# Optimization experiments

Measured on AMD Instinct MI355X. Metric: run time of the kernel, lower is better.

## Reference

```python
import jax, jax.numpy as jnp
import numpy as np

K, L = 9, 32


def conv1d(x, w):
    # x: [b, C, P], w: [O, C, 3]; padding=1 kernel=3 == SAME
    return jax.lax.conv_general_dilated(
        x, w, window_strides=(1,), padding='SAME',
        dimension_numbers=('NCH', 'OIH', 'NCH'))


def prior_surface(x, w1, w2, w3, w4):
    # x: [b, P]
    h = jax.nn.relu(conv1d(x[:, None, :], w1))
    h = jax.nn.relu(conv1d(h, w2))
    h = jax.nn.relu(conv1d(h, w3))
    out = x[:, None, :] + jax.nn.relu(conv1d(h, w4))
    return jnp.clip(out, 0.0, 1.0)[:, 0, :]


def setup_inputs() -> dict:
    key = jax.random.key(0)
    ks = jax.random.split(key, 9)
    b, E, M, P = 32, 20, 64, 3072
    d_split = 0.1 * jax.random.normal(ks[0], (b, E, M), jnp.float32)
    surf0 = jax.random.uniform(ks[1], (b, P), dtype=jnp.float32)
    clouds0 = jax.random.uniform(ks[2], (b, E, P), dtype=jnp.float32)
    # scale Phi so gradients stay in a sane range for the [0,1] clamps
    Phi_split = jax.random.normal(ks[3], (b, E, M, P), jnp.float32) / P
    rho_base = 0.1 * jax.random.uniform(ks[4], (b,), dtype=jnp.float32)
    rho = jnp.ones((K,), jnp.float32)

    def kaiming(k, shape):
        fan_in = shape[-2] * shape[-1]
        return jax.random.normal(k, shape, jnp.float32) * np.float32(np.sqrt(2.0 / fan_in))

    w1 = kaiming(ks[5], (K, L, 1, 3))
    w2 = kaiming(ks[6], (K, L, L, 3))
    w3 = kaiming(ks[7], (K, L, L, 3))
    w4 = kaiming(ks[8], (K, 1, L, 3))
    return {"d_split": d_split, "surf0": surf0, "clouds0": clouds0,
            "Phi_split": Phi_split, "rho_base": rho_base, "rho": rho,
            "w1": w1, "w2": w2, "w3": w3, "w4": w4, "n_epochs": 20}


def reference(d_split, surf0, clouds0, Phi_split, rho_base, rho, w1, w2, w3, w4, n_epochs):
    # d_split: [b,E,M], surf0: [b,P], clouds0: [b,E,P], Phi_split: [b,E,M,P], rho_base: [b]
    surf, clouds = surf0, clouds0
    out_surface, out_clouds = [], []
    for i in range(K):
        t0 = 1.0 - clouds                       # [b,E,P]
        t1 = t0 * t0
        tmp = clouds + t1 * surf[:, None, :]    # [b,E,P]
        y = jnp.einsum('bemp,bep->bem', Phi_split, tmp)          # Phi @ tmp
        t2 = jnp.einsum('bemp,bem->bep', Phi_split, y - d_split)  # PhiT @ resid
        # the torch loop over j accumulates grad_surf += 2*t2*t1; equivalent sum over E
        grad_surf = surf0 + 2.0 * jnp.sum(t2 * t1, axis=1)        # [b,P]
        grad_clouds = 2.0 * t2 - 4.0 * t2 * surf[:, None, :] * t0 # [b,E,P]
        rho_i = jnp.clip(rho[i], 0.1, 3.0)
        r_surf = surf - rho_base[:, None] * rho_i * grad_surf
        r_clouds = clouds - rho_base[:, None, None] * rho_i * grad_clouds
        surf = prior_surface(r_surf, w1[i], w2[i], w3[i], w4[i])
        clouds = jax.nn.relu(r_clouds)
        out_surface.append(surf)
        out_clouds.append(clouds)
    return (surf, clouds, jnp.stack(out_surface), jnp.stack(out_clouds))
```

## Files before the change

kernel.cpp:

```cpp
#include <hip/hip_runtime.h>

#define B_ 32
#define E_ 20
#define M_ 64
#define P_ 3072
#define K_ 9
#define TT 384
#define NT (P_ / TT)

#define PHI_SCALE 65536.0f
#define PHI_INV   (1.0f / 65536.0f)

typedef float floatx2 __attribute__((ext_vector_type(2)));

__device__ __forceinline__ unsigned int pack4_fp8(float f0, float f1, float f2, float f3)
{
    int w = 0;
    w = __builtin_amdgcn_cvt_pk_fp8_f32(f0, f1, w, false);
    w = __builtin_amdgcn_cvt_pk_fp8_f32(f2, f3, w, true);
    return (unsigned int)w;
}

template <int MODE>
__global__ __launch_bounds__(256) void k_y(
    const float* __restrict__ PhiF,
    const unsigned char* __restrict__ Phi8,
    unsigned char* __restrict__ Phi8out,
    const float* __restrict__ dsplit,
    const float* __restrict__ surf_cur,
    const float* __restrict__ clouds_cur,
    float* __restrict__ yr)
{
    __shared__ float s_tmp[P_];
    const int bid = blockIdx.x >> 1;
    const int mh  = blockIdx.x & 1;
    const int b   = bid / E_;
    const int tid = threadIdx.x;

    const float4* cl4 = reinterpret_cast<const float4*>(clouds_cur + (size_t)bid * P_);
    const float4* sf4 = reinterpret_cast<const float4*>(surf_cur + (size_t)b * P_);
    for (int f = tid; f < P_ / 4; f += 256) {
        float4 c4 = cl4[f], s4 = sf4[f], tm;
        float t0x = 1.f - c4.x, t0y = 1.f - c4.y, t0z = 1.f - c4.z, t0w = 1.f - c4.w;
        tm.x = c4.x + t0x * t0x * s4.x;
        tm.y = c4.y + t0y * t0y * s4.y;
        tm.z = c4.z + t0z * t0z * s4.z;
        tm.w = c4.w + t0w * t0w * s4.w;
        reinterpret_cast<float4*>(s_tmp)[f] = tm;
    }
    __syncthreads();

    const int wave = tid >> 6, lane = tid & 63;
    const size_t base = (size_t)bid * (M_ * P_);

    #pragma unroll
    for (int r = 0; r < 8; ++r) {
        const int mg = mh * 32 + wave * 8 + r;
        float acc = 0.f;
        if constexpr (MODE != 2) {
            const float4* prow = reinterpret_cast<const float4*>(PhiF + base + (size_t)mg * P_);
            unsigned int* orow = reinterpret_cast<unsigned int*>(Phi8out + base + (size_t)mg * P_);
            #pragma unroll
            for (int j = 0; j < 12; ++j) {
                const int f = j * 64 + lane;
                float4 v = prow[f];
                float4 t = reinterpret_cast<const float4*>(s_tmp)[f];
                acc += v.x * t.x + v.y * t.y + v.z * t.z + v.w * t.w;
                if constexpr (MODE == 1) {
                    orow[f] = pack4_fp8(v.x * PHI_SCALE, v.y * PHI_SCALE,
                                        v.z * PHI_SCALE, v.w * PHI_SCALE);
                }
            }
        } else {
            const uint2* prow = reinterpret_cast<const uint2*>(Phi8 + base + (size_t)mg * P_);
            #pragma unroll
            for (int j = 0; j < 6; ++j) {
                const int f = j * 64 + lane;
                uint2 w = prow[f];
                floatx2 l0 = __builtin_amdgcn_cvt_pk_f32_fp8((int)w.x, false);
                floatx2 h0 = __builtin_amdgcn_cvt_pk_f32_fp8((int)w.x, true);
                floatx2 l1 = __builtin_amdgcn_cvt_pk_f32_fp8((int)w.y, false);
                floatx2 h1 = __builtin_amdgcn_cvt_pk_f32_fp8((int)w.y, true);
                float4 a = reinterpret_cast<const float4*>(s_tmp)[2 * f];
                float4 bb = reinterpret_cast<const float4*>(s_tmp)[2 * f + 1];
                acc += l0.x * a.x + l0.y * a.y + h0.x * a.z + h0.y * a.w
                     + l1.x * bb.x + l1.y * bb.y + h1.x * bb.z + h1.y * bb.w;
            }
        }
        #pragma unroll
        for (int off = 32; off > 0; off >>= 1)
            acc += __shfl_down(acc, off, 64);
        if (lane == 0) {
            if constexpr (MODE == 2) acc *= PHI_INV;
            yr[bid * M_ + mg] = acc - dsplit[bid * M_ + mg];
        }
    }
}

__global__ __launch_bounds__(192) void k_t2_f8(
    const unsigned char* __restrict__ Phi8,
    const float* __restrict__ yr,
    const float* __restrict__ surf_cur,
    const float* __restrict__ clouds_cur,
    const float* __restrict__ rho_base,
    const float* __restrict__ rho_i,
    float* __restrict__ s2t1,
    float* __restrict__ out_clouds_i)
{
    __shared__ float s_yr[M_];
    const int bid = blockIdx.x >> 1;
    const int ph  = blockIdx.x & 1;
    const int b   = bid / E_;
    const int tid = threadIdx.x;

    if (tid < M_) s_yr[tid] = yr[bid * M_ + tid];
    __syncthreads();

    const int p0 = ph * 1536 + tid * 8;
    const unsigned char* phi = Phi8 + (size_t)bid * (M_ * P_) + p0;

    float acc[8] = {0.f, 0.f, 0.f, 0.f, 0.f, 0.f, 0.f, 0.f};
    #pragma unroll 8
    for (int m = 0; m < M_; ++m) {
        const float ym = s_yr[m];
        uint2 w = *reinterpret_cast<const uint2*>(phi + (size_t)m * P_);
        floatx2 l0 = __builtin_amdgcn_cvt_pk_f32_fp8((int)w.x, false);
        floatx2 h0 = __builtin_amdgcn_cvt_pk_f32_fp8((int)w.x, true);
        floatx2 l1 = __builtin_amdgcn_cvt_pk_f32_fp8((int)w.y, false);
        floatx2 h1 = __builtin_amdgcn_cvt_pk_f32_fp8((int)w.y, true);
        acc[0] += l0.x * ym; acc[1] += l0.y * ym; acc[2] += h0.x * ym; acc[3] += h0.y * ym;
        acc[4] += l1.x * ym; acc[5] += l1.y * ym; acc[6] += h1.x * ym; acc[7] += h1.y * ym;
    }
    #pragma unroll
    for (int k = 0; k < 8; ++k) acc[k] *= PHI_INV;

    const float s = rho_base[b] * fminf(fmaxf(*rho_i, 0.1f), 3.0f);
    const size_t gi = (size_t)bid * P_ + p0;
    float4 c0 = *reinterpret_cast<const float4*>(clouds_cur + gi);
    float4 c1 = *reinterpret_cast<const float4*>(clouds_cur + gi + 4);
    const size_t si = (size_t)b * P_ + p0;
    float4 v0 = *reinterpret_cast<const float4*>(surf_cur + si);
    float4 v1 = *reinterpret_cast<const float4*>(surf_cur + si + 4);

    float cl[8] = {c0.x, c0.y, c0.z, c0.w, c1.x, c1.y, c1.z, c1.w};
    float sv[8] = {v0.x, v0.y, v0.z, v0.w, v1.x, v1.y, v1.z, v1.w};
    float st[8], nc[8];
    #pragma unroll
    for (int k = 0; k < 8; ++k) {
        float t0 = 1.f - cl[k];
        st[k] = acc[k] * t0 * t0;
        float gc = 2.f * acc[k] * (1.f - 2.f * sv[k] * t0);
        nc[k] = fmaxf(cl[k] - s * gc, 0.f);
    }
    reinterpret_cast<float4*>(s2t1 + gi)[0] = make_float4(st[0], st[1], st[2], st[3]);
    reinterpret_cast<float4*>(s2t1 + gi + 4)[0] = make_float4(st[4], st[5], st[6], st[7]);
    reinterpret_cast<float4*>(out_clouds_i + gi)[0] = make_float4(nc[0], nc[1], nc[2], nc[3]);
    reinterpret_cast<float4*>(out_clouds_i + gi + 4)[0] = make_float4(nc[4], nc[5], nc[6], nc[7]);
}

__global__ __launch_bounds__(192) void k_t2_f32(
    const float* __restrict__ Phi,
    const float* __restrict__ yr,
    const float* __restrict__ surf_cur,
    const float* __restrict__ clouds_cur,
    const float* __restrict__ rho_base,
    const float* __restrict__ rho_i,
    float* __restrict__ s2t1,
    float* __restrict__ out_clouds_i)
{
    __shared__ float s_yr[M_];
    const int bid = blockIdx.x >> 1;
    const int ph  = blockIdx.x & 1;
    const int b   = bid / E_;
    const int tid = threadIdx.x;

    if (tid < M_) s_yr[tid] = yr[bid * M_ + tid];
    __syncthreads();

    const int p0 = ph * 1536 + tid * 8;
    const float* phi = Phi + (size_t)bid * (M_ * P_) + p0;

    float acc[8] = {0.f, 0.f, 0.f, 0.f, 0.f, 0.f, 0.f, 0.f};
    #pragma unroll 4
    for (int m = 0; m < M_; ++m) {
        const float ym = s_yr[m];
        float4 a = *reinterpret_cast<const float4*>(phi + (size_t)m * P_);
        float4 bv = *reinterpret_cast<const float4*>(phi + (size_t)m * P_ + 4);
        acc[0] += a.x * ym; acc[1] += a.y * ym; acc[2] += a.z * ym; acc[3] += a.w * ym;
        acc[4] += bv.x * ym; acc[5] += bv.y * ym; acc[6] += bv.z * ym; acc[7] += bv.w * ym;
    }

    const float s = rho_base[b] * fminf(fmaxf(*rho_i, 0.1f), 3.0f);
    const size_t gi = (size_t)bid * P_ + p0;
    float4 c0 = *reinterpret_cast<const float4*>(clouds_cur + gi);
    float4 c1 = *reinterpret_cast<const float4*>(clouds_cur + gi + 4);
    const size_t si = (size_t)b * P_ + p0;
    float4 v0 = *reinterpret_cast<const float4*>(surf_cur + si);
    float4 v1 = *reinterpret_cast<const float4*>(surf_cur + si + 4);

    float cl[8] = {c0.x, c0.y, c0.z, c0.w, c1.x, c1.y, c1.z, c1.w};
    float sv[8] = {v0.x, v0.y, v0.z, v0.w, v1.x, v1.y, v1.z, v1.w};
    float st[8], nc[8];
    #pragma unroll
    for (int k = 0; k < 8; ++k) {
        float t0 = 1.f - cl[k];
        st[k] = acc[k] * t0 * t0;
        float gc = 2.f * acc[k] * (1.f - 2.f * sv[k] * t0);
        nc[k] = fmaxf(cl[k] - s * gc, 0.f);
    }
    reinterpret_cast<float4*>(s2t1 + gi)[0] = make_float4(st[0], st[1], st[2], st[3]);
    reinterpret_cast<float4*>(s2t1 + gi + 4)[0] = make_float4(st[4], st[5], st[6], st[7]);
    reinterpret_cast<float4*>(out_clouds_i + gi)[0] = make_float4(nc[0], nc[1], nc[2], nc[3]);
    reinterpret_cast<float4*>(out_clouds_i + gi + 4)[0] = make_float4(nc[4], nc[5], nc[6], nc[7]);
}

__device__ __forceinline__ void conv32_rt(const float* __restrict__ inb,
                                          float* __restrict__ outb,
                                          const float* __restrict__ w,
                                          const int Wout, const int pstart)
{
    const int tid = threadIdx.x;
    const int QG = (Wout + 3) >> 2;
    const int items = 8 * QG;
    for (int g = tid; g < items; g += 256) {
        const int oo = g / QG;
        const int q  = g - oo * QG;
        const int j0 = q << 2;
        float a[4][4];
        #pragma unroll
        for (int ol = 0; ol < 4; ++ol)
            a[ol][0] = a[ol][1] = a[ol][2] = a[ol][3] = 0.f;
        #pragma unroll 4
        for (int c = 0; c < 32; ++c) {
            const float* ip = inb + c * 400 + j0;
            const float4 i03 = *reinterpret_cast<const float4*>(ip);
            const float2 i45 = *reinterpret_cast<const float2*>(ip + 4);
            const float* wb = w + (c * 32 + oo * 4) * 4;
            #pragma unroll
            for (int ol = 0; ol < 4; ++ol) {
                const float4 wv = *reinterpret_cast<const float4*>(wb + ol * 4);
                a[ol][0] += i03.x * wv.x + i03.y * wv.y + i03.z * wv.z;
                a[ol][1] += i03.y * wv.x + i03.z * wv.y + i03.w * wv.z;
                a[ol][2] += i03.z * wv.x + i03.w * wv.y + i45.x * wv.z;
                a[ol][3] += i03.w * wv.x + i45.x * wv.y + i45.y * wv.z;
            }
        }
        const int p = pstart + j0;
        #pragma unroll
        for (int ol = 0; ol < 4; ++ol) {
            float* op = outb + (oo * 4 + ol) * 400 + j0;
            if (j0     < Wout) op[0] = (p     >= 0 && p     < P_) ? fmaxf(a[ol][0], 0.f) : 0.f;
            if (j0 + 1 < Wout) op[1] = (p + 1 >= 0 && p + 1 < P_) ? fmaxf(a[ol][1], 0.f) : 0.f;
            if (j0 + 2 < Wout) op[2] = (p + 2 >= 0 && p + 2 < P_) ? fmaxf(a[ol][2], 0.f) : 0.f;
            if (j0 + 3 < Wout) op[3] = (p + 3 >= 0 && p + 3 < P_) ? fmaxf(a[ol][3], 0.f) : 0.f;
        }
    }
}

__global__ __launch_bounds__(256) void k_surf(
    const float* __restrict__ surf0,
    const float* __restrict__ surf_cur,
    const float* __restrict__ s2t1,
    const float* __restrict__ rho_base,
    const float* __restrict__ rho_i,
    const float* __restrict__ w1,
    const float* __restrict__ w2,
    const float* __restrict__ w3,
    const float* __restrict__ w4,
    float* __restrict__ out_surface_i)
{
    __shared__ float sx[400];
    __shared__ float bufA[32 * 400];
    __shared__ float bufB[32 * 400];
    __shared__ float sw2s[32 * 32 * 4];
    __shared__ float sw3s[32 * 32 * 4];
    __shared__ float sw1s[32 * 4];
    __shared__ float sw4s[32 * 4];

    const int tid = threadIdx.x;
    const int b  = blockIdx.x / NT;
    const int t  = blockIdx.x % NT;
    const int p0 = t * TT;

    for (int i = tid; i < 1024; i += 256) {
        const int c = i >> 5, o = i & 31;
        const int src = (o * 32 + c) * 3;
        sw2s[i * 4 + 0] = w2[src + 0];
        sw2s[i * 4 + 1] = w2[src + 1];
        sw2s[i * 4 + 2] = w2[src + 2];
        sw2s[i * 4 + 3] = 0.f;
        sw3s[i * 4 + 0] = w3[src + 0];
        sw3s[i * 4 + 1] = w3[src + 1];
        sw3s[i * 4 + 2] = w3[src + 2];
        sw3s[i * 4 + 3] = 0.f;
    }
    if (tid < 32) {
        sw1s[tid * 4 + 0] = w1[tid * 3 + 0];
        sw1s[tid * 4 + 1] = w1[tid * 3 + 1];
        sw1s[tid * 4 + 2] = w1[tid * 3 + 2];
        sw1s[tid * 4 + 3] = 0.f;
        sw4s[tid * 4 + 0] = w4[tid * 3 + 0];
        sw4s[tid * 4 + 1] = w4[tid * 3 + 1];
        sw4s[tid * 4 + 2] = w4[tid * 3 + 2];
        sw4s[tid * 4 + 3] = 0.f;
    }
    for (int i = tid; i < 32 * 16; i += 256) {
        const int c = i >> 4, j = 384 + (i & 15);
        bufA[c * 400 + j] = 0.f;
        bufB[c * 400 + j] = 0.f;
    }

    const float s = rho_base[b] * fminf(fmaxf(*rho_i, 0.1f), 3.0f);

    for (int j = tid; j < 400; j += 256) {
        float v = 0.f;
        const int p = p0 + j - 4;
        if (j < TT + 8 && p >= 0 && p < P_) {
            float g = surf0[(size_t)b * P_ + p];
            #pragma unroll
            for (int e = 0; e < E_; ++e)
                g += 2.f * s2t1[((size_t)(b * E_ + e)) * P_ + p];
            v = surf_cur[(size_t)b * P_ + p] - s * g;
        }
        sx[j] = v;
    }
    __syncthreads();

    {
        const int Wout = TT + 6;
        const int QG = (Wout + 3) >> 2;
        const int pstart = p0 - 3;
        for (int g = tid; g < 32 * QG; g += 256) {
            const int o = g / QG;
            const int q = g - o * QG;
            const int j0 = q << 2;
            const float4 i03 = *reinterpret_cast<const float4*>(&sx[j0]);
            const float2 i45 = *reinterpret_cast<const float2*>(&sx[j0 + 4]);
            const float4 wv = *reinterpret_cast<const float4*>(&sw1s[o * 4]);
            float a0 = i03.x * wv.x + i03.y * wv.y + i03.z * wv.z;
            float a1 = i03.y * wv.x + i03.z * wv.y + i03.w * wv.z;
            float a2 = i03.z * wv.x + i03.w * wv.y + i45.x * wv.z;
            float a3 = i03.w * wv.x + i45.x * wv.y + i45.y * wv.z;
            float* op = &bufA[o * 400 + j0];
            const int p = pstart + j0;
            if (j0     < Wout) op[0] = (p     >= 0 && p     < P_) ? fmaxf(a0, 0.f) : 0.f;
            if (j0 + 1 < Wout) op[1] = (p + 1 >= 0 && p + 1 < P_) ? fmaxf(a1, 0.f) : 0.f;
            if (j0 + 2 < Wout) op[2] = (p + 2 >= 0 && p + 2 < P_) ? fmaxf(a2, 0.f) : 0.f;
            if (j0 + 3 < Wout) op[3] = (p + 3 >= 0 && p + 3 < P_) ? fmaxf(a3, 0.f) : 0.f;
        }
    }
    __syncthreads();
    conv32_rt(bufA, bufB, sw2s, TT + 4, p0 - 2);
    __syncthreads();
    conv32_rt(bufB, bufA, sw3s, TT + 2, p0 - 1);
    __syncthreads();

    for (int g = tid; g < TT / 4; g += 256) {
        const int j0 = g << 2;
        float a0 = 0.f, a1 = 0.f, a2 = 0.f, a3 = 0.f;
        #pragma unroll 8
        for (int c = 0; c < 32; ++c) {
            const float* ip = &bufA[c * 400 + j0];
            const float4 i03 = *reinterpret_cast<const float4*>(ip);
            const float2 i45 = *reinterpret_cast<const float2*>(ip + 4);
            const float4 wv = *reinterpret_cast<const float4*>(&sw4s[c * 4]);
            a0 += i03.x * wv.x + i03.y * wv.y + i03.z * wv.z;
            a1 += i03.y * wv.x + i03.z * wv.y + i03.w * wv.z;
            a2 += i03.z * wv.x + i03.w * wv.y + i45.x * wv.z;
            a3 += i03.w * wv.x + i45.x * wv.y + i45.y * wv.z;
        }
        const float4 xr = *reinterpret_cast<const float4*>(&sx[j0 + 4]);
        float4 ov;
        ov.x = fminf(fmaxf(xr.x + fmaxf(a0, 0.f), 0.f), 1.f);
        ov.y = fminf(fmaxf(xr.y + fmaxf(a1, 0.f), 0.f), 1.f);
        ov.z = fminf(fmaxf(xr.z + fmaxf(a2, 0.f), 0.f), 1.f);
        ov.w = fminf(fmaxf(xr.w + fmaxf(a3, 0.f), 0.f), 1.f);
        *reinterpret_cast<float4*>(&out_surface_i[(size_t)b * P_ + p0 + j0]) = ov;
    }
}

extern "C" void kernel_launch(void* const* d_in, const int* in_sizes, int n_in,
                              void* d_out, int out_size, void* d_ws, size_t ws_size,
                              hipStream_t stream)
{
    (void)in_sizes; (void)n_in; (void)out_size;

    const float* dsplit   = (const float*)d_in[0];
    const float* surf0    = (const float*)d_in[1];
    const float* clouds0  = (const float*)d_in[2];
    const float* Phi      = (const float*)d_in[3];
    const float* rho_base = (const float*)d_in[4];
    const float* rho      = (const float*)d_in[5];
    const float* w1       = (const float*)d_in[6];
    const float* w2       = (const float*)d_in[7];
    const float* w3       = (const float*)d_in[8];
    const float* w4       = (const float*)d_in[9];

    float* out = (float*)d_out;
    float* out_surf_final   = out;
    float* out_clouds_final = out + (size_t)B_ * P_;
    float* out_surface      = out_clouds_final + (size_t)B_ * E_ * P_;
    float* out_clouds       = out_surface + (size_t)K_ * B_ * P_;

    float* yr   = out_surf_final;
    float* s2t1 = out_clouds_final;

    const size_t PHI_N = (size_t)B_ * E_ * M_ * P_;
    const bool use8 = (ws_size >= PHI_N);
    unsigned char* phi8 = (unsigned char*)d_ws;

    for (int i = 0; i < K_; ++i) {
        const float* scur = (i == 0) ? surf0   : out_surface + (size_t)(i - 1) * B_ * P_;
        const float* ccur = (i == 0) ? clouds0 : out_clouds + (size_t)(i - 1) * B_ * E_ * P_;
        float* oc_i = out_clouds + (size_t)i * B_ * E_ * P_;

        if (use8) {
            if (i == 0)
                k_y<1><<<dim3(B_ * E_ * 2), dim3(256), 0, stream>>>(
                    Phi, nullptr, phi8, dsplit, scur, ccur, yr);
            else
                k_y<2><<<dim3(B_ * E_ * 2), dim3(256), 0, stream>>>(
                    nullptr, phi8, nullptr, dsplit, scur, ccur, yr);
            k_t2_f8<<<dim3(B_ * E_ * 2), dim3(192), 0, stream>>>(
                phi8, yr, scur, ccur, rho_base, rho + i, s2t1, oc_i);
        } else {
            k_y<0><<<dim3(B_ * E_ * 2), dim3(256), 0, stream>>>(
                Phi, nullptr, nullptr, dsplit, scur, ccur, yr);
            k_t2_f32<<<dim3(B_ * E_ * 2), dim3(192), 0, stream>>>(
                Phi, yr, scur, ccur, rho_base, rho + i, s2t1, oc_i);
        }

        k_surf<<<dim3(B_ * NT), dim3(256), 0, stream>>>(
            surf0, scur, s2t1, rho_base, rho + i,
            w1 + (size_t)i * 96, w2 + (size_t)i * 3072,
            w3 + (size_t)i * 3072, w4 + (size_t)i * 96,
            out_surface + (size_t)i * B_ * P_);
    }

    hipMemcpyAsync(out_surf_final, out_surface + (size_t)(K_ - 1) * B_ * P_,
                   (size_t)B_ * P_ * sizeof(float), hipMemcpyDeviceToDevice, stream);
    hipMemcpyAsync(out_clouds_final, out_clouds + (size_t)(K_ - 1) * B_ * E_ * P_,
                   (size_t)B_ * E_ * P_ * sizeof(float), hipMemcpyDeviceToDevice, stream);
}
```

Before: 1.050 ms.

## Fuse Phi forward and transpose products into one kernel, retile surface conv

```diff
diff --git a/kernel.cpp b/kernel.cpp
--- a/kernel.cpp
+++ b/kernel.cpp
@@ -5,13 +5,16 @@
 #define M_ 64
 #define P_ 3072
 #define K_ 9
-#define TT 384
-#define NT (P_ / TT)
+#define BEP (B_ * E_ * P_)
+#define TT2 192
+#define NT2 16
+#define BUFW 208
 
 #define PHI_SCALE 65536.0f
 #define PHI_INV   (1.0f / 65536.0f)
 
 typedef float floatx2 __attribute__((ext_vector_type(2)));
+typedef _Float16 half4v __attribute__((ext_vector_type(4)));
 
 __device__ __forceinline__ unsigned int pack4_fp8(float f0, float f1, float f2, float f3)
 {
@@ -22,57 +25,74 @@
 }
 
 template <int MODE>
-__global__ __launch_bounds__(256) void k_y(
+__global__ __launch_bounds__(256) void k_A(
     const float* __restrict__ PhiF,
     const unsigned char* __restrict__ Phi8,
-    unsigned char* __restrict__ Phi8out,
+    unsigned char* __restrict__ Phi8w,
     const float* __restrict__ dsplit,
     const float* __restrict__ surf_cur,
     const float* __restrict__ clouds_cur,
-    float* __restrict__ yr)
+    const float* __restrict__ rho_base,
+    const float* __restrict__ rho_i,
+    float* __restrict__ s2t1,
+    float* __restrict__ out_clouds_i,
+    float* __restrict__ out_clouds_final)
 {
     __shared__ float s_tmp[P_];
-    const int bid = blockIdx.x >> 1;
-    const int mh  = blockIdx.x & 1;
+    __shared__ float s_yr[M_];
+
+    const int bid = blockIdx.x;
     const int b   = bid / E_;
     const int tid = threadIdx.x;
-
-    const float4* cl4 = reinterpret_cast<const float4*>(clouds_cur + (size_t)bid * P_);
-    const float4* sf4 = reinterpret_cast<const float4*>(surf_cur + (size_t)b * P_);
-    for (int f = tid; f < P_ / 4; f += 256) {
-        float4 c4 = cl4[f], s4 = sf4[f], tm;
-        float t0x = 1.f - c4.x, t0y = 1.f - c4.y, t0z = 1.f - c4.z, t0w = 1.f - c4.w;
-        tm.x = c4.x + t0x * t0x * s4.x;
-        tm.y = c4.y + t0y * t0y * s4.y;
-        tm.z = c4.z + t0z * t0z * s4.z;
-        tm.w = c4.w + t0w * t0w * s4.w;
-        reinterpret_cast<float4*>(s_tmp)[f] = tm;
-    }
-    __syncthreads();
-
     const int wave = tid >> 6, lane = tid & 63;
     const size_t base = (size_t)bid * (M_ * P_);
 
-    #pragma unroll
-    for (int r = 0; r < 8; ++r) {
-        const int mg = mh * 32 + wave * 8 + r;
-        float acc = 0.f;
-        if constexpr (MODE != 2) {
+    const float* ccur = clouds_cur + (size_t)bid * P_;
+    const float* scur = surf_cur + (size_t)b * P_;
+
+    {
+        const float4* cl4 = reinterpret_cast<const float4*>(ccur);
+        const float4* sf4 = reinterpret_cast<const float4*>(scur);
+        for (int f = tid; f < P_ / 4; f += 256) {
+            float4 c4 = cl4[f], s4 = sf4[f], tm;
+            float t0x = 1.f - c4.x, t0y = 1.f - c4.y, t0z = 1.f - c4.z, t0w = 1.f - c4.w;
+            tm.x = c4.x + t0x * t0x * s4.x;
+            tm.y = c4.y + t0y * t0y * s4.y;
+            tm.z = c4.z + t0z * t0z * s4.z;
+            tm.w = c4.w + t0w * t0w * s4.w;
+            reinterpret_cast<float4*>(s_tmp)[f] = tm;
+        }
+    }
+    __syncthreads();
+
+    if constexpr (MODE == 0) {
+        #pragma unroll 2
+        for (int r = 0; r < 16; ++r) {
+            const int mg = (wave << 4) + r;
             const float4* prow = reinterpret_cast<const float4*>(PhiF + base + (size_t)mg * P_);
-            unsigned int* orow = reinterpret_cast<unsigned int*>(Phi8out + base + (size_t)mg * P_);
+            unsigned int* orow = reinterpret_cast<unsigned int*>(Phi8w + base + (size_t)mg * P_);
+            float acc = 0.f;
             #pragma unroll
             for (int j = 0; j < 12; ++j) {
                 const int f = j * 64 + lane;
                 float4 v = prow[f];
                 float4 t = reinterpret_cast<const float4*>(s_tmp)[f];
                 acc += v.x * t.x + v.y * t.y + v.z * t.z + v.w * t.w;
-                if constexpr (MODE == 1) {
-                    orow[f] = pack4_fp8(v.x * PHI_SCALE, v.y * PHI_SCALE,
-                                        v.z * PHI_SCALE, v.w * PHI_SCALE);
-                }
-            }
-        } else {
+                orow[f] = pack4_fp8(v.x * PHI_SCALE, v.y * PHI_SCALE,
+                                    v.z * PHI_SCALE, v.w * PHI_SCALE);
+            }
+            #pragma unroll
+            for (int off = 32; off > 0; off >>= 1)
+                acc += __shfl_down(acc, off, 64);
+            if (lane == 0)
+                s_yr[mg] = acc - dsplit[bid * M_ + mg];
+        }
+    } else {
+        #pragma unroll 2
+        for (int r = 0; r < 16; ++r) {
+            const int mg = (wave << 4) + r;
             const uint2* prow = reinterpret_cast<const uint2*>(Phi8 + base + (size_t)mg * P_);
+            float acc = 0.f;
             #pragma unroll
             for (int j = 0; j < 6; ++j) {
                 const int f = j * 64 + lane;
@@ -81,178 +101,65 @@
                 floatx2 h0 = __builtin_amdgcn_cvt_pk_f32_fp8((int)w.x, true);
                 floatx2 l1 = __builtin_amdgcn_cvt_pk_f32_fp8((int)w.y, false);
                 floatx2 h1 = __builtin_amdgcn_cvt_pk_f32_fp8((int)w.y, true);
-                float4 a = reinterpret_cast<const float4*>(s_tmp)[2 * f];
-                float4 bb = reinterpret_cast<const float4*>(s_tmp)[2 * f + 1];
+                const float4 a  = reinterpret_cast<const float4*>(s_tmp)[2 * f];
+                const float4 bb = reinterpret_cast<const float4*>(s_tmp)[2 * f + 1];
                 acc += l0.x * a.x + l0.y * a.y + h0.x * a.z + h0.y * a.w
                      + l1.x * bb.x + l1.y * bb.y + h1.x * bb.z + h1.y * bb.w;
             }
-        }
+            #pragma unroll
+            for (int off = 32; off > 0; off >>= 1)
+                acc += __shfl_down(acc, off, 64);
+            if (lane == 0)
+                s_yr[mg] = acc * PHI_INV - dsplit[bid * M_ + mg];
+        }
+    }
+    __syncthreads();
+
+    {
+        const unsigned char* p8 = ((MODE == 0) ? Phi8w : Phi8) + base + tid * 12;
+        float acc[12];
         #pragma unroll
-        for (int off = 32; off > 0; off >>= 1)
-            acc += __shfl_down(acc, off, 64);
-        if (lane == 0) {
-            if constexpr (MODE == 2) acc *= PHI_INV;
-            yr[bid * M_ + mg] = acc - dsplit[bid * M_ + mg];
-        }
-    }
-}
-
-__global__ __launch_bounds__(192) void k_t2_f8(
-    const unsigned char* __restrict__ Phi8,
-    const float* __restrict__ yr,
-    const float* __restrict__ surf_cur,
-    const float* __restrict__ clouds_cur,
-    const float* __restrict__ rho_base,
-    const float* __restrict__ rho_i,
-    float* __restrict__ s2t1,
-    float* __restrict__ out_clouds_i)
-{
-    __shared__ float s_yr[M_];
-    const int bid = blockIdx.x >> 1;
-    const int ph  = blockIdx.x & 1;
-    const int b   = bid / E_;
-    const int tid = threadIdx.x;
-
-    if (tid < M_) s_yr[tid] = yr[bid * M_ + tid];
-    __syncthreads();
-
-    const int p0 = ph * 1536 + tid * 8;
-    const unsigned char* phi = Phi8 + (size_t)bid * (M_ * P_) + p0;
-
-    float acc[8] = {0.f, 0.f, 0.f, 0.f, 0.f, 0.f, 0.f, 0.f};
-    #pragma unroll 8
-    for (int m = 0; m < M_; ++m) {
-        const float ym = s_yr[m];
-        uint2 w = *reinterpret_cast<const uint2*>(phi + (size_t)m * P_);
-        floatx2 l0 = __builtin_amdgcn_cvt_pk_f32_fp8((int)w.x, false);
-        floatx2 h0 = __builtin_amdgcn_cvt_pk_f32_fp8((int)w.x, true);
-        floatx2 l1 = __builtin_amdgcn_cvt_pk_f32_fp8((int)w.y, false);
-        floatx2 h1 = __builtin_amdgcn_cvt_pk_f32_fp8((int)w.y, true);
-        acc[0] += l0.x * ym; acc[1] += l0.y * ym; acc[2] += h0.x * ym; acc[3] += h0.y * ym;
-        acc[4] += l1.x * ym; acc[5] += l1.y * ym; acc[6] += h1.x * ym; acc[7] += h1.y * ym;
-    }
-    #pragma unroll
-    for (int k = 0; k < 8; ++k) acc[k] *= PHI_INV;
-
-    const float s = rho_base[b] * fminf(fmaxf(*rho_i, 0.1f), 3.0f);
-    const size_t gi = (size_t)bid * P_ + p0;
-    float4 c0 = *reinterpret_cast<const float4*>(clouds_cur + gi);
-    float4 c1 = *reinterpret_cast<const float4*>(clouds_cur + gi + 4);
-    const size_t si = (size_t)b * P_ + p0;
-    float4 v0 = *reinterpret_cast<const float4*>(surf_cur + si);
-    float4 v1 = *reinterpret_cast<const float4*>(surf_cur + si + 4);
-
-    float cl[8] = {c0.x, c0.y, c0.z, c0.w, c1.x, c1.y, c1.z, c1.w};
-    float sv[8] = {v0.x, v0.y, v0.z, v0.w, v1.x, v1.y, v1.z, v1.w};
-    float st[8], nc[8];
-    #pragma unroll
-    for (int k = 0; k < 8; ++k) {
-        float t0 = 1.f - cl[k];
-        st[k] = acc[k] * t0 * t0;
-        float gc = 2.f * acc[k] * (1.f - 2.f * sv[k] * t0);
-        nc[k] = fmaxf(cl[k] - s * gc, 0.f);
-    }
-    reinterpret_cast<float4*>(s2t1 + gi)[0] = make_float4(st[0], st[1], st[2], st[3]);
-    reinterpret_cast<float4*>(s2t1 + gi + 4)[0] = make_float4(st[4], st[5], st[6], st[7]);
-    reinterpret_cast<float4*>(out_clouds_i + gi)[0] = make_float4(nc[0], nc[1], nc[2], nc[3]);
-    reinterpret_cast<float4*>(out_clouds_i + gi + 4)[0] = make_float4(nc[4], nc[5], nc[6], nc[7]);
-}
-
-__global__ __launch_bounds__(192) void k_t2_f32(
-    const float* __restrict__ Phi,
-    const float* __restrict__ yr,
-    const float* __restrict__ surf_cur,
-    const float* __restrict__ clouds_cur,
-    const float* __restrict__ rho_base,
-    const float* __restrict__ rho_i,
-    float* __restrict__ s2t1,
-    float* __restrict__ out_clouds_i)
-{
-    __shared__ float s_yr[M_];
-    const int bid = blockIdx.x >> 1;
-    const int ph  = blockIdx.x & 1;
-    const int b   = bid / E_;
-    const int tid = threadIdx.x;
-
-    if (tid < M_) s_yr[tid] = yr[bid * M_ + tid];
-    __syncthreads();
-
-    const int p0 = ph * 1536 + tid * 8;
-    const float* phi = Phi + (size_t)bid * (M_ * P_) + p0;
-
-    float acc[8] = {0.f, 0.f, 0.f, 0.f, 0.f, 0.f, 0.f, 0.f};
-    #pragma unroll 4
-    for (int m = 0; m < M_; ++m) {
-        const float ym = s_yr[m];
-        float4 a = *reinterpret_cast<const float4*>(phi + (size_t)m * P_);
-        float4 bv = *reinterpret_cast<const float4*>(phi + (size_t)m * P_ + 4);
-        acc[0] += a.x * ym; acc[1] += a.y * ym; acc[2] += a.z * ym; acc[3] += a.w * ym;
-        acc[4] += bv.x * ym; acc[5] += bv.y * ym; acc[6] += bv.z * ym; acc[7] += bv.w * ym;
-    }
-
-    const float s = rho_base[b] * fminf(fmaxf(*rho_i, 0.1f), 3.0f);
-    const size_t gi = (size_t)bid * P_ + p0;
-    float4 c0 = *reinterpret_cast<const float4*>(clouds_cur + gi);
-    float4 c1 = *reinterpret_cast<const float4*>(clouds_cur + gi + 4);
-    const size_t si = (size_t)b * P_ + p0;
-    float4 v0 = *reinterpret_cast<const float4*>(surf_cur + si);
-    float4 v1 = *reinterpret_cast<const float4*>(surf_cur + si + 4);
-
-    float cl[8] = {c0.x, c0.y, c0.z, c0.w, c1.x, c1.y, c1.z, c1.w};
-    float sv[8] = {v0.x, v0.y, v0.z, v0.w, v1.x, v1.y, v1.z, v1.w};
-    float st[8], nc[8];
-    #pragma unroll
-    for (int k = 0; k < 8; ++k) {
-        float t0 = 1.f - cl[k];
-        st[k] = acc[k] * t0 * t0;
-        float gc = 2.f * acc[k] * (1.f - 2.f * sv[k] * t0);
-        nc[k] = fmaxf(cl[k] - s * gc, 0.f);
-    }
-    reinterpret_cast<float4*>(s2t1 + gi)[0] = make_float4(st[0], st[1], st[2], st[3]);
-    reinterpret_cast<float4*>(s2t1 + gi + 4)[0] = make_float4(st[4], st[5], st[6], st[7]);
-    reinterpret_cast<float4*>(out_clouds_i + gi)[0] = make_float4(nc[0], nc[1], nc[2], nc[3]);
-    reinterpret_cast<float4*>(out_clouds_i + gi + 4)[0] = make_float4(nc[4], nc[5], nc[6], nc[7]);
-}
-
-__device__ __forceinline__ void conv32_rt(const float* __restrict__ inb,
-                                          float* __restrict__ outb,
-                                          const float* __restrict__ w,
-                                          const int Wout, const int pstart)
-{
-    const int tid = threadIdx.x;
-    const int QG = (Wout + 3) >> 2;
-    const int items = 8 * QG;
-    for (int g = tid; g < items; g += 256) {
-        const int oo = g / QG;
-        const int q  = g - oo * QG;
-        const int j0 = q << 2;
-        float a[4][4];
+        for (int k = 0; k < 12; ++k) acc[k] = 0.f;
+        #pragma unroll 4
+        for (int m = 0; m < M_; ++m) {
+            const float ym = s_yr[m];
+            uint3 w = *reinterpret_cast<const uint3*>(p8 + (size_t)m * P_);
+            floatx2 c0 = __builtin_amdgcn_cvt_pk_f32_fp8((int)w.x, false);
+            floatx2 c1 = __builtin_amdgcn_cvt_pk_f32_fp8((int)w.x, true);
+            floatx2 c2 = __builtin_amdgcn_cvt_pk_f32_fp8((int)w.y, false);
+            floatx2 c3 = __builtin_amdgcn_cvt_pk_f32_fp8((int)w.y, true);
+            floatx2 c4 = __builtin_amdgcn_cvt_pk_f32_fp8((int)w.z, false);
+            floatx2 c5 = __builtin_amdgcn_cvt_pk_f32_fp8((int)w.z, true);
+            acc[0] += c0.x * ym; acc[1]  += c0.y * ym;
+            acc[2] += c1.x * ym; acc[3]  += c1.y * ym;
+            acc[4] += c2.x * ym; acc[5]  += c2.y * ym;
+            acc[6] += c3.x * ym; acc[7]  += c3.y * ym;
+            acc[8] += c4.x * ym; acc[9]  += c4.y * ym;
+            acc[10]+= c5.x * ym; acc[11] += c5.y * ym;
+        }
+
+        const float s = rho_base[b] * fminf(fmaxf(*rho_i, 0.1f), 3.0f);
+        const int p0t = tid * 12;
+        const size_t gi = (size_t)bid * P_ + p0t;
         #pragma unroll
-        for (int ol = 0; ol < 4; ++ol)
-            a[ol][0] = a[ol][1] = a[ol][2] = a[ol][3] = 0.f;
-        #pragma unroll 4
-        for (int c = 0; c < 32; ++c) {
-            const float* ip = inb + c * 400 + j0;
-            const float4 i03 = *reinterpret_cast<const float4*>(ip);
-            const float2 i45 = *reinterpret_cast<const float2*>(ip + 4);
-            const float* wb = w + (c * 32 + oo * 4) * 4;
-            #pragma unroll
-            for (int ol = 0; ol < 4; ++ol) {
-                const float4 wv = *reinterpret_cast<const float4*>(wb + ol * 4);
-                a[ol][0] += i03.x * wv.x + i03.y * wv.y + i03.z * wv.z;
-                a[ol][1] += i03.y * wv.x + i03.z * wv.y + i03.w * wv.z;
-                a[ol][2] += i03.z * wv.x + i03.w * wv.y + i45.x * wv.z;
-                a[ol][3] += i03.w * wv.x + i45.x * wv.y + i45.y * wv.z;
-            }
-        }
-        const int p = pstart + j0;
-        #pragma unroll
-        for (int ol = 0; ol < 4; ++ol) {
-            float* op = outb + (oo * 4 + ol) * 400 + j0;
-            if (j0     < Wout) op[0] = (p     >= 0 && p     < P_) ? fmaxf(a[ol][0], 0.f) : 0.f;
-            if (j0 + 1 < Wout) op[1] = (p + 1 >= 0 && p + 1 < P_) ? fmaxf(a[ol][1], 0.f) : 0.f;
-            if (j0 + 2 < Wout) op[2] = (p + 2 >= 0 && p + 2 < P_) ? fmaxf(a[ol][2], 0.f) : 0.f;
-            if (j0 + 3 < Wout) op[3] = (p + 3 >= 0 && p + 3 < P_) ? fmaxf(a[ol][3], 0.f) : 0.f;
+        for (int k4 = 0; k4 < 3; ++k4) {
+            float4 cv = *reinterpret_cast<const float4*>(ccur + p0t + k4 * 4);
+            float4 sv = *reinterpret_cast<const float4*>(scur + p0t + k4 * 4);
+            float4 stv, ncv;
+#define EPI(C, KK)                                                      \
+            {                                                           \
+                float t2v = acc[k4 * 4 + KK] * PHI_INV;                 \
+                float t0  = 1.f - cv.C;                                 \
+                stv.C = t2v * t0 * t0;                                  \
+                float gc = 2.f * t2v * (1.f - 2.f * sv.C * t0);         \
+                ncv.C = fmaxf(cv.C - s * gc, 0.f);                      \
+            }
+            EPI(x, 0) EPI(y, 1) EPI(z, 2) EPI(w, 3)
+#undef EPI
+            *reinterpret_cast<float4*>(s2t1 + gi + k4 * 4) = stv;
+            *reinterpret_cast<float4*>(out_clouds_i + gi + k4 * 4) = ncv;
+            if (out_clouds_final)
+                *reinterpret_cast<float4*>(out_clouds_final + gi + k4 * 4) = ncv;
         }
     }
 }
@@ -267,32 +174,33 @@
     const float* __restrict__ w2,
     const float* __restrict__ w3,
     const float* __restrict__ w4,
-    float* __restrict__ out_surface_i)
+    float* __restrict__ out_surface_i,
+    float* __restrict__ out_surf_final)
 {
-    __shared__ float sx[400];
-    __shared__ float bufA[32 * 400];
-    __shared__ float bufB[32 * 400];
-    __shared__ float sw2s[32 * 32 * 4];
-    __shared__ float sw3s[32 * 32 * 4];
+    __shared__ float sx[BUFW];
+    __shared__ float bufA[32 * BUFW];
+    __shared__ float bufB[32 * BUFW];
+    __shared__ _Float16 sw2h[32 * 32 * 4];
+    __shared__ _Float16 sw3h[32 * 32 * 4];
     __shared__ float sw1s[32 * 4];
     __shared__ float sw4s[32 * 4];
 
     const int tid = threadIdx.x;
-    const int b  = blockIdx.x / NT;
-    const int t  = blockIdx.x % NT;
-    const int p0 = t * TT;
-
-    for (int i = tid; i < 1024; i += 256) {
-        const int c = i >> 5, o = i & 31;
+    const int b  = blockIdx.x >> 4;
+    const int p0 = (blockIdx.x & 15) * TT2;
+    const size_t bP = (size_t)b * P_;
+
+    for (int idx = tid; idx < 1024; idx += 256) {
+        const int c = idx >> 5, o = idx & 31;
         const int src = (o * 32 + c) * 3;
-        sw2s[i * 4 + 0] = w2[src + 0];
-        sw2s[i * 4 + 1] = w2[src + 1];
-        sw2s[i * 4 + 2] = w2[src + 2];
-        sw2s[i * 4 + 3] = 0.f;
-        sw3s[i * 4 + 0] = w3[src + 0];
-        sw3s[i * 4 + 1] = w3[src + 1];
-        sw3s[i * 4 + 2] = w3[src + 2];
-        sw3s[i * 4 + 3] = 0.f;
+        sw2h[idx * 4 + 0] = (_Float16)w2[src + 0];
+        sw2h[idx * 4 + 1] = (_Float16)w2[src + 1];
+        sw2h[idx * 4 + 2] = (_Float16)w2[src + 2];
+        sw2h[idx * 4 + 3] = (_Float16)0.f;
+        sw3h[idx * 4 + 0] = (_Float16)w3[src + 0];
+        sw3h[idx * 4 + 1] = (_Float16)w3[src + 1];
+        sw3h[idx * 4 + 2] = (_Float16)w3[src + 2];
+        sw3h[idx * 4 + 3] = (_Float16)0.f;
     }
     if (tid < 32) {
         sw1s[tid * 4 + 0] = w1[tid * 3 + 0];
@@ -304,36 +212,29 @@
         sw4s[tid * 4 + 2] = w4[tid * 3 + 2];
         sw4s[tid * 4 + 3] = 0.f;
     }
-    for (int i = tid; i < 32 * 16; i += 256) {
-        const int c = i >> 4, j = 384 + (i & 15);
-        bufA[c * 400 + j] = 0.f;
-        bufB[c * 400 + j] = 0.f;
-    }
 
     const float s = rho_base[b] * fminf(fmaxf(*rho_i, 0.1f), 3.0f);
 
-    for (int j = tid; j < 400; j += 256) {
+    for (int j = tid; j < BUFW; j += 256) {
         float v = 0.f;
         const int p = p0 + j - 4;
-        if (j < TT + 8 && p >= 0 && p < P_) {
-            float g = surf0[(size_t)b * P_ + p];
+        if (j < TT2 + 8 && p >= 0 && p < P_) {
+            float g = surf0[bP + p];
             #pragma unroll
             for (int e = 0; e < E_; ++e)
                 g += 2.f * s2t1[((size_t)(b * E_ + e)) * P_ + p];
-            v = surf_cur[(size_t)b * P_ + p] - s * g;
+            v = surf_cur[bP + p] - s * g;
         }
         sx[j] = v;
     }
     __syncthreads();
 
     {
-        const int Wout = TT + 6;
-        const int QG = (Wout + 3) >> 2;
+        const int Wout = TT2 + 6;
+        const int QG = 50;
         const int pstart = p0 - 3;
         for (int g = tid; g < 32 * QG; g += 256) {
-            const int o = g / QG;
-            const int q = g - o * QG;
-            const int j0 = q << 2;
+            const int o = g / QG, q = g - o * QG, j0 = q << 2;
             const float4 i03 = *reinterpret_cast<const float4*>(&sx[j0]);
             const float2 i45 = *reinterpret_cast<const float2*>(&sx[j0 + 4]);
             const float4 wv = *reinterpret_cast<const float4*>(&sw1s[o * 4]);
@@ -341,7 +242,7 @@
             float a1 = i03.y * wv.x + i03.z * wv.y + i03.w * wv.z;
             float a2 = i03.z * wv.x + i03.w * wv.y + i45.x * wv.z;
             float a3 = i03.w * wv.x + i45.x * wv.y + i45.y * wv.z;
-            float* op = &bufA[o * 400 + j0];
+            float* op = &bufA[o * BUFW + j0];
             const int p = pstart + j0;
             if (j0     < Wout) op[0] = (p     >= 0 && p     < P_) ? fmaxf(a0, 0.f) : 0.f;
             if (j0 + 1 < Wout) op[1] = (p + 1 >= 0 && p + 1 < P_) ? fmaxf(a1, 0.f) : 0.f;
@@ -350,32 +251,73 @@
         }
     }
     __syncthreads();
-    conv32_rt(bufA, bufB, sw2s, TT + 4, p0 - 2);
-    __syncthreads();
-    conv32_rt(bufB, bufA, sw3s, TT + 2, p0 - 1);
-    __syncthreads();
-
-    for (int g = tid; g < TT / 4; g += 256) {
-        const int j0 = g << 2;
-        float a0 = 0.f, a1 = 0.f, a2 = 0.f, a3 = 0.f;
-        #pragma unroll 8
-        for (int c = 0; c < 32; ++c) {
-            const float* ip = &bufA[c * 400 + j0];
-            const float4 i03 = *reinterpret_cast<const float4*>(ip);
-            const float2 i45 = *reinterpret_cast<const float2*>(ip + 4);
-            const float4 wv = *reinterpret_cast<const float4*>(&sw4s[c * 4]);
-            a0 += i03.x * wv.x + i03.y * wv.y + i03.z * wv.z;
-            a1 += i03.y * wv.x + i03.z * wv.y + i03.w * wv.z;
-            a2 += i03.z * wv.x + i03.w * wv.y + i45.x * wv.z;
-            a3 += i03.w * wv.x + i45.x * wv.y + i45.y * wv.z;
-        }
-        const float4 xr = *reinterpret_cast<const float4*>(&sx[j0 + 4]);
-        float4 ov;
-        ov.x = fminf(fmaxf(xr.x + fmaxf(a0, 0.f), 0.f), 1.f);
-        ov.y = fminf(fmaxf(xr.y + fmaxf(a1, 0.f), 0.f), 1.f);
-        ov.z = fminf(fmaxf(xr.z + fmaxf(a2, 0.f), 0.f), 1.f);
-        ov.w = fminf(fmaxf(xr.w + fmaxf(a3, 0.f), 0.f), 1.f);
-        *reinterpret_cast<float4*>(&out_surface_i[(size_t)b * P_ + p0 + j0]) = ov;
+
+    for (int layer = 0; layer < 2; ++layer) {
+        const float* inb  = layer ? bufB : bufA;
+        float* outb       = layer ? bufA : bufB;
+        const _Float16* w = layer ? sw3h : sw2h;
+        const int Wout    = layer ? (TT2 + 2) : (TT2 + 4);
+        const int pstart  = layer ? (p0 - 1) : (p0 - 2);
+        const int QG = (Wout + 3) >> 2;
+        for (int g = tid; g < 8 * QG; g += 256) {
+            const int oo = g / QG, q = g - oo * QG, j0 = q << 2;
+            float a[4][4];
+            #pragma unroll
+            for (int ol = 0; ol < 4; ++ol)
+                a[ol][0] = a[ol][1] = a[ol][2] = a[ol][3] = 0.f;
+            #pragma unroll 4
+            for (int c = 0; c < 32; ++c) {
+                const float* ip = inb + c * BUFW + j0;
+                const float4 i03 = *reinterpret_cast<const float4*>(ip);
+                const float2 i45 = *reinterpret_cast<const float2*>(ip + 4);
+                const float f0 = i03.x, f1 = i03.y, f2 = i03.z,
+                            f3 = i03.w, f4 = i45.x, f5 = i45.y;
+                const _Float16* wb = w + (c * 32 + oo * 4) * 4;
+                #pragma unroll
+                for (int ol = 0; ol < 4; ++ol) {
+                    half4v wv = *reinterpret_cast<const half4v*>(wb + ol * 4);
+                    const float w0 = wv[0], w1v = wv[1], w2v = wv[2];
+                    a[ol][0] += f0 * w0 + f1 * w1v + f2 * w2v;
+                    a[ol][1] += f1 * w0 + f2 * w1v + f3 * w2v;
+                    a[ol][2] += f2 * w0 + f3 * w1v + f4 * w2v;
+                    a[ol][3] += f3 * w0 + f4 * w1v + f5 * w2v;
+                }
+            }
+            const int p = pstart + j0;
+            #pragma unroll
+            for (int ol = 0; ol < 4; ++ol) {
+                float* op = outb + (oo * 4 + ol) * BUFW + j0;
+                if (j0     < Wout) op[0] = (p     >= 0 && p     < P_) ? fmaxf(a[ol][0], 0.f) : 0.f;
+                if (j0 + 1 < Wout) op[1] = (p + 1 >= 0 && p + 1 < P_) ? fmaxf(a[ol][1], 0.f) : 0.f;
+                if (j0 + 2 < Wout) op[2] = (p + 2 >= 0 && p + 2 < P_) ? fmaxf(a[ol][2], 0.f) : 0.f;
+                if (j0 + 3 < Wout) op[3] = (p + 3 >= 0 && p + 3 < P_) ? fmaxf(a[ol][3], 0.f) : 0.f;
+            }
+        }
+        __syncthreads();
+    }
+
+    {
+        float* orow = out_surface_i + bP + p0;
+        for (int g = tid; g < TT2 / 2; g += 256) {
+            const int j0 = g * 2;
+            float a0 = 0.f, a1 = 0.f;
+            #pragma unroll 8
+            for (int c = 0; c < 32; ++c) {
+                const float* ip = &bufA[c * BUFW + j0];
+                const float2 iA = *reinterpret_cast<const float2*>(ip);
+                const float2 iB = *reinterpret_cast<const float2*>(ip + 2);
+                const float4 wv = *reinterpret_cast<const float4*>(&sw4s[c * 4]);
+                a0 += iA.x * wv.x + iA.y * wv.y + iB.x * wv.z;
+                a1 += iA.y * wv.x + iB.x * wv.y + iB.y * wv.z;
+            }
+            const float x0 = sx[j0 + 4], x1 = sx[j0 + 5];
+            float2 ov;
+            ov.x = fminf(fmaxf(x0 + fmaxf(a0, 0.f), 0.f), 1.f);
+            ov.y = fminf(fmaxf(x1 + fmaxf(a1, 0.f), 0.f), 1.f);
+            *reinterpret_cast<float2*>(orow + j0) = ov;
+            if (out_surf_final)
+                *reinterpret_cast<float2*>(out_surf_final + bP + p0 + j0) = ov;
+        }
     }
 }
 
@@ -383,7 +325,7 @@
                               void* d_out, int out_size, void* d_ws, size_t ws_size,
                               hipStream_t stream)
 {
-    (void)in_sizes; (void)n_in; (void)out_size;
+    (void)in_sizes; (void)n_in; (void)out_size; (void)ws_size;
 
     const float* dsplit   = (const float*)d_in[0];
     const float* surf0    = (const float*)d_in[1];
@@ -399,46 +341,32 @@
     float* out = (float*)d_out;
     float* out_surf_final   = out;
     float* out_clouds_final = out + (size_t)B_ * P_;
-    float* out_surface      = out_clouds_final + (size_t)B_ * E_ * P_;
+    float* out_surface      = out_clouds_final + (size_t)BEP;
     float* out_clouds       = out_surface + (size_t)K_ * B_ * P_;
 
-    float* yr   = out_surf_final;
-    float* s2t1 = out_clouds_final;
-
-    const size_t PHI_N = (size_t)B_ * E_ * M_ * P_;
-    const bool use8 = (ws_size >= PHI_N);
     unsigned char* phi8 = (unsigned char*)d_ws;
+    float* s2t1 = (float*)((unsigned char*)d_ws + (size_t)B_ * E_ * M_ * P_);
 
     for (int i = 0; i < K_; ++i) {
         const float* scur = (i == 0) ? surf0   : out_surface + (size_t)(i - 1) * B_ * P_;
-        const float* ccur = (i == 0) ? clouds0 : out_clouds + (size_t)(i - 1) * B_ * E_ * P_;
-        float* oc_i = out_clouds + (size_t)i * B_ * E_ * P_;
-
-        if (use8) {
-            if (i == 0)
-                k_y<1><<<dim3(B_ * E_ * 2), dim3(256), 0, stream>>>(
-                    Phi, nullptr, phi8, dsplit, scur, ccur, yr);
-            else
-                k_y<2><<<dim3(B_ * E_ * 2), dim3(256), 0, stream>>>(
-                    nullptr, phi8, nullptr, dsplit, scur, ccur, yr);
-            k_t2_f8<<<dim3(B_ * E_ * 2), dim3(192), 0, stream>>>(
-                phi8, yr, scur, ccur, rho_base, rho + i, s2t1, oc_i);
-        } else {
-            k_y<0><<<dim3(B_ * E_ * 2), dim3(256), 0, stream>>>(
-                Phi, nullptr, nullptr, dsplit, scur, ccur, yr);
-            k_t2_f32<<<dim3(B_ * E_ * 2), dim3(192), 0, stream>>>(
-                Phi, yr, scur, ccur, rho_base, rho + i, s2t1, oc_i);
-        }
-
-        k_surf<<<dim3(B_ * NT), dim3(256), 0, stream>>>(
+        const float* ccur = (i == 0) ? clouds0 : out_clouds + (size_t)(i - 1) * BEP;
+        float* oc_i = out_clouds + (size_t)i * BEP;
+        float* ocF  = (i == K_ - 1) ? out_clouds_final : nullptr;
+        float* osF  = (i == K_ - 1) ? out_surf_final : nullptr;
+
+        if (i == 0)
+            k_A<0><<<dim3(B_ * E_), dim3(256), 0, stream>>>(
+                Phi, nullptr, phi8, dsplit, scur, ccur,
+                rho_base, rho + i, s2t1, oc_i, ocF);
+        else
+            k_A<1><<<dim3(B_ * E_), dim3(256), 0, stream>>>(
+                nullptr, phi8, nullptr, dsplit, scur, ccur,
+                rho_base, rho + i, s2t1, oc_i, ocF);
+
+        k_surf<<<dim3(B_ * NT2), dim3(256), 0, stream>>>(
             surf0, scur, s2t1, rho_base, rho + i,
             w1 + (size_t)i * 96, w2 + (size_t)i * 3072,
             w3 + (size_t)i * 3072, w4 + (size_t)i * 96,
-            out_surface + (size_t)i * B_ * P_);
-    }
-
-    hipMemcpyAsync(out_surf_final, out_surface + (size_t)(K_ - 1) * B_ * P_,
-                   (size_t)B_ * P_ * sizeof(float), hipMemcpyDeviceToDevice, stream);
-    hipMemcpyAsync(out_clouds_final, out_clouds + (size_t)(K_ - 1) * B_ * E_ * P_,
-                   (size_t)B_ * E_ * P_ * sizeof(float), hipMemcpyDeviceToDevice, stream);
+            out_surface + (size_t)i * B_ * P_, osF);
+    }
 }
```

New measurement: 904.6 us. 1.16x faster.
